# Kernel tuning notes

Hardware: AMD Instinct MI355X
Metric: run time of the kernel (lower is better)

## Reference

```python
import jax, jax.numpy as jnp
import numpy as np

STRIDES = (8, 16, 32, 64, 128)
LEVEL_HW = ((128, 160), (64, 80), (32, 40), (16, 20), (8, 10))
IMG_H, IMG_W = 1024, 1280
B, NUM_CLASSES = 16, 20
SCORE_THR, IOU_THR, MAX_DET = 0.05, 0.6, 1000


def _coords_all():
    # coords_fmap2orig for every level, concatenated -> [N, 2] (x, y)
    cs = []
    for (h, w), s in zip(LEVEL_HW, STRIDES):
        sx = jnp.arange(w, dtype=jnp.float32) * s + s // 2
        sy = jnp.arange(h, dtype=jnp.float32) * s + s // 2
        yy, xx = jnp.meshgrid(sy, sx, indexing='ij')
        cs.append(jnp.stack([xx.reshape(-1), yy.reshape(-1)], -1))
    return jnp.concatenate(cs, 0)


def _reshape_cat(levels):
    # list of [B,C,h,w] -> [B, sum(h*w), C]
    return jnp.concatenate(
        [p.transpose(0, 2, 3, 1).reshape(p.shape[0], -1, p.shape[1]) for p in levels], 1)


def _decode(cls_l, cnt_l, reg_l, coords):
    cls = jax.nn.sigmoid(_reshape_cat(cls_l))           # [B,N,C]
    cnt = jax.nn.sigmoid(_reshape_cat(cnt_l))[..., 0]   # [B,N]
    reg = _reshape_cat(reg_l)                           # [B,N,4] ltrb
    scores = jnp.sqrt(jnp.max(cls, -1) * cnt)           # add_centerness + sqrt
    classes = jnp.argmax(cls, -1) + 1
    boxes = jnp.concatenate([coords[None] - reg[..., :2], coords[None] + reg[..., 2:]], -1)
    return scores, classes, boxes


def _nms_keep(boxes, scores, classes, valid):
    # masked greedy per-class NMS on fixed size M; returns keep mask [M]
    boxes = jax.lax.stop_gradient(boxes)
    scores = jax.lax.stop_gradient(scores)
    maxc = jnp.max(jnp.where(valid[:, None], boxes, 0.0))
    b = boxes + (classes.astype(boxes.dtype) * (maxc + 1.0))[:, None]  # class offsets
    order = jnp.argsort(-jnp.where(valid, scores, -jnp.inf))
    b = b[order]
    v = valid[order]
    x1, y1, x2, y2 = b[:, 0], b[:, 1], b[:, 2], b[:, 3]
    areas = (x2 - x1 + 1.0) * (y2 - y1 + 1.0)
    iw = jnp.clip(jnp.minimum(x2[:, None], x2[None, :]) - jnp.maximum(x1[:, None], x1[None, :]) + 1.0, 0.0)
    ih = jnp.clip(jnp.minimum(y2[:, None], y2[None, :]) - jnp.maximum(y1[:, None], y1[None, :]) + 1.0, 0.0)
    inter = iw * ih
    iou = inter / (areas[:, None] + areas[None, :] - inter)
    M = boxes.shape[0]

    def body(i, carry):
        keep, sup = carry
        k = v[i] & (~sup[i])
        keep = keep.at[i].set(k)
        sup = sup | (k & (iou[i] > IOU_THR))
        return keep, sup

    keep_s, _ = jax.lax.fori_loop(0, M, body, (jnp.zeros(M, bool), jnp.zeros(M, bool)))
    return jnp.zeros(M, bool).at[order].set(keep_s)


def _forward(args):
    cls_r, cnt_r, reg_r = args[0:5], args[5:10], args[10:15]
    cls_i, cnt_i, reg_i = args[15:20], args[20:25], args[25:30]
    coords = _coords_all()
    s_r, c_r, b_r = _decode(cls_r, cnt_r, reg_r, coords)
    s_i, c_i, b_i = _decode(cls_i, cnt_i, reg_i, coords)
    scores = jnp.concatenate([s_r, s_i], 1)   # [B, 2N]
    classes = jnp.concatenate([c_r, c_i], 1)
    boxes = jnp.concatenate([b_r, b_i], 1)
    top_s, top_i = jax.lax.top_k(scores, MAX_DET)
    top_c = jnp.take_along_axis(classes, top_i, 1)
    top_b = jnp.take_along_axis(boxes, top_i[..., None], 1)
    valid = top_s >= SCORE_THR
    keep = jax.vmap(_nms_keep)(top_b, top_s, top_c, valid)
    # ClipBoxes: clamp to image bounds
    top_b = jnp.maximum(top_b, 0.0)
    xs = jnp.minimum(top_b[..., 0::2], IMG_W - 1.0)
    ys = jnp.minimum(top_b[..., 1::2], IMG_H - 1.0)
    top_b = jnp.stack([xs[..., 0], ys[..., 0], xs[..., 1], ys[..., 1]], -1)
    kf = keep.astype(top_s.dtype)
    return top_s * kf, top_c * keep, top_b * kf[..., None], keep


def setup_inputs() -> dict:
    key = jax.random.key(0)
    chans = {'cls': NUM_CLASSES, 'cnt': 1, 'reg': 4}
    inp = {}
    i = 0
    for mod in ('r', 'i'):
        for kind in ('cls', 'cnt', 'reg'):
            for l, (h, w) in enumerate(LEVEL_HW):
                k = jax.random.fold_in(key, i); i += 1
                inp[f'{kind}_{mod}_{l}'] = jax.random.normal(k, (B, chans[kind], h, w), jnp.float32)
    return inp


def reference(cls_r_0, cls_r_1, cls_r_2, cls_r_3, cls_r_4,
              cnt_r_0, cnt_r_1, cnt_r_2, cnt_r_3, cnt_r_4,
              reg_r_0, reg_r_1, reg_r_2, reg_r_3, reg_r_4,
              cls_i_0, cls_i_1, cls_i_2, cls_i_3, cls_i_4,
              cnt_i_0, cnt_i_1, cnt_i_2, cnt_i_3, cnt_i_4,
              reg_i_0, reg_i_1, reg_i_2, reg_i_3, reg_i_4):
    args = [cls_r_0, cls_r_1, cls_r_2, cls_r_3, cls_r_4,
            cnt_r_0, cnt_r_1, cnt_r_2, cnt_r_3, cnt_r_4,
            reg_r_0, reg_r_1, reg_r_2, reg_r_3, reg_r_4,
            cls_i_0, cls_i_1, cls_i_2, cls_i_3, cls_i_4,
            cnt_i_0, cnt_i_1, cnt_i_2, cnt_i_3, cnt_i_4,
            reg_i_0, reg_i_1, reg_i_2, reg_i_3, reg_i_4]
    return _forward(args)
```

## Files before the change

kernel.cpp:

```cpp
#include <hip/hip_runtime.h>
#include <hip/hip_bf16.h>

typedef unsigned long long u64;
typedef unsigned int u32;

#define NTOT    54560
#define NMOD    27280
#define BATCH   16
#define KPAD    1024
#define MAXD    1000
#define NBIN    16384
#define CAND    6144
#define NCHUNK  7

struct Ptrs { const float* p[30]; };

constexpr size_t SZ_KEY    = (size_t)BATCH * NTOT * 8;
constexpr size_t SZ_TOPK   = (size_t)BATCH * KPAD * 8;
constexpr size_t SZ_TRAW   = (size_t)BATCH * KPAD * 16;
constexpr size_t SZ_T1     = (size_t)BATCH * KPAD * 4;
constexpr size_t SZ_MAXC   = (size_t)BATCH * 32 * 4;
constexpr size_t SZ_VALID  = (size_t)BATCH * 32 * 4;
constexpr size_t SZ_MASK   = (size_t)BATCH * KPAD * 32 * 4;
constexpr size_t SZ_GHIST  = (size_t)BATCH * NBIN * 4;
constexpr size_t SZ_GHISTP = (size_t)BATCH * NCHUNK * NBIN * 4;
constexpr size_t SZ_GB1    = 256;
constexpr size_t SZ_GCAND  = (size_t)BATCH * CAND * 8;

constexpr size_t OFF_KEY    = 0;
constexpr size_t OFF_TOPK   = OFF_KEY   + SZ_KEY;
constexpr size_t OFF_TRAW   = OFF_TOPK  + SZ_TOPK;
constexpr size_t OFF_TSCORE = OFF_TRAW  + SZ_TRAW;
constexpr size_t OFF_TCLSF  = OFF_TSCORE+ SZ_T1;
constexpr size_t OFF_MAXC   = OFF_TCLSF + SZ_T1;
constexpr size_t OFF_VALID  = OFF_MAXC  + SZ_MAXC;
constexpr size_t OFF_MASK   = OFF_VALID + SZ_VALID;
constexpr size_t OFF_GHIST  = OFF_MASK  + SZ_MASK;
constexpr size_t OFF_GHISTP = OFF_GHIST + SZ_GHIST;
constexpr size_t OFF_GB1    = OFF_GHISTP+ SZ_GHISTP;
constexpr size_t OFF_GCAND  = OFF_GB1   + SZ_GB1;

__device__ inline void level_of(int nm, int& l, int& pos, int& w, int& s, int& hw) {
    if (nm < 20480)      { l = 0; pos = nm;         w = 160; s = 8;   hw = 20480; }
    else if (nm < 25600) { l = 1; pos = nm - 20480; w = 80;  s = 16;  hw = 5120; }
    else if (nm < 26880) { l = 2; pos = nm - 25600; w = 40;  s = 32;  hw = 1280; }
    else if (nm < 27200) { l = 3; pos = nm - 26880; w = 20;  s = 64;  hw = 320; }
    else                 { l = 4; pos = nm - 27200; w = 10;  s = 128; hw = 80; }
}

__device__ inline float sigm(float x) { return 1.0f / (1.0f + expf(-x)); }

__device__ inline void ld_lds16(const float* g, float* l) {
    __builtin_amdgcn_global_load_lds(
        (const __attribute__((address_space(1))) void*)g,
        (__attribute__((address_space(3))) void*)l, 16, 0, 0);
}

__global__ __launch_bounds__(128)
void decode_kernel(Ptrs ptrs, u64* __restrict__ keyAll) {
    __shared__ float lds[21 * 512];
    int cc = blockIdx.x;
    int b = blockIdx.y;

    if (cc >= 100) {
        int t = (cc - 100) * 128 + threadIdx.x;
        if (t >= 3360) return;
        int mod = t / 1680;
        int tm = t % 1680;
        int q = t & 3;
        int nm = 25600 + (tm & ~3);
        int l, pos, w, s, hw;
        level_of(nm, l, pos, w, s, hw);
        (void)w; (void)s;
        const float* clsP = ptrs.p[mod * 15 + l];
        const float* cntP = ptrs.p[mod * 15 + 5 + l];
        const float4* cb = (const float4*)(clsP + (size_t)b * 20 * hw + pos);
        int hw4 = hw >> 2;
        int c0 = q * 5;
        float4 v[5];
        #pragma unroll
        for (int c = 0; c < 5; ++c) v[c] = cb[(size_t)(c0 + c) * hw4];
        float4 cv = *(const float4*)(cntP + (size_t)b * hw + pos);
        float4 mx = v[0];
        #pragma unroll
        for (int c = 1; c < 5; ++c) {
            mx.x = fmaxf(mx.x, v[c].x); mx.y = fmaxf(mx.y, v[c].y);
            mx.z = fmaxf(mx.z, v[c].z); mx.w = fmaxf(mx.w, v[c].w);
        }
        mx.x = fmaxf(mx.x, __shfl_xor(mx.x, 1));
        mx.y = fmaxf(mx.y, __shfl_xor(mx.y, 1));
        mx.z = fmaxf(mx.z, __shfl_xor(mx.z, 1));
        mx.w = fmaxf(mx.w, __shfl_xor(mx.w, 1));
        mx.x = fmaxf(mx.x, __shfl_xor(mx.x, 2));
        mx.y = fmaxf(mx.y, __shfl_xor(mx.y, 2));
        mx.z = fmaxf(mx.z, __shfl_xor(mx.z, 2));
        mx.w = fmaxf(mx.w, __shfl_xor(mx.w, 2));
        float ma = (q & 1) ? ((q & 2) ? mx.w : mx.y) : ((q & 2) ? mx.z : mx.x);
        float ca = (q & 1) ? ((q & 2) ? cv.w : cv.y) : ((q & 2) ? cv.z : cv.x);
        u32 sb = __float_as_uint(sqrtf(__fmul_rn(sigm(ma), sigm(ca))));
        int n = mod * NMOD + nm + q;
        keyAll[(size_t)b * NTOT + n] = ((u64)sb << 16) | (u64)(65535 - n);
        return;
    }

    int mod = cc / 50, c = cc % 50;
    int l     = (c < 40) ? 0 : 1;
    int hw    = (c < 40) ? 20480 : 5120;
    int pos0  = (c < 40) ? c * 512 : (c - 40) * 512;
    int nmb   = (l == 0) ? pos0 : 20480 + pos0;
    const float* clsP = ptrs.p[mod * 15 + l];
    const float* cntP = ptrs.p[mod * 15 + 5 + l];
    int wave = threadIdx.x >> 6, lane = threadIdx.x & 63;

    const float* cbase = clsP + (size_t)b * 20 * hw + pos0 + wave * 256 + lane * 4;
    float* dbase = lds + wave * 256;
    #pragma unroll
    for (int ch = 0; ch < 20; ++ch)
        ld_lds16(cbase + (size_t)ch * hw, dbase + ch * 512);
    ld_lds16(cntP + (size_t)b * hw + pos0 + wave * 256 + lane * 4, dbase + 20 * 512);
    __syncthreads();

    int t = threadIdx.x;
    const float4* l4 = (const float4*)lds;
    float4 mx = l4[t];
    #pragma unroll
    for (int ch = 1; ch < 20; ++ch) {
        float4 v = l4[ch * 128 + t];
        mx.x = fmaxf(mx.x, v.x); mx.y = fmaxf(mx.y, v.y);
        mx.z = fmaxf(mx.z, v.z); mx.w = fmaxf(mx.w, v.w);
    }
    float4 cv = l4[20 * 128 + t];

    int n = mod * NMOD + nmb + t * 4;
    u32 s0 = __float_as_uint(sqrtf(__fmul_rn(sigm(mx.x), sigm(cv.x))));
    u32 s1 = __float_as_uint(sqrtf(__fmul_rn(sigm(mx.y), sigm(cv.y))));
    u32 s2 = __float_as_uint(sqrtf(__fmul_rn(sigm(mx.z), sigm(cv.z))));
    u32 s3 = __float_as_uint(sqrtf(__fmul_rn(sigm(mx.w), sigm(cv.w))));
    ulonglong2* ka2 = (ulonglong2*)(keyAll + (size_t)b * NTOT + n);
    ulonglong2 k01, k23;
    k01.x = ((u64)s0 << 16) | (u64)(65535 - n);
    k01.y = ((u64)s1 << 16) | (u64)(65535 - (n + 1));
    k23.x = ((u64)s2 << 16) | (u64)(65535 - (n + 2));
    k23.y = ((u64)s3 << 16) | (u64)(65535 - (n + 3));
    ka2[0] = k01; ka2[1] = k23;
}

__global__ __launch_bounds__(1024)
void hist_kernel(const u64* __restrict__ keyAll, u32* __restrict__ ghistP,
                 u32* __restrict__ maxcG) {
    __shared__ u32 shist[NBIN];
    int b = blockIdx.y, chunk = blockIdx.x, tid = threadIdx.x;
    #pragma unroll
    for (int j = 0; j < NBIN / 1024; ++j) shist[tid + j * 1024] = 0u;
    if (chunk == 0 && tid == 0) maxcG[b * 32] = 0u;
    __syncthreads();

    const u64* keys = keyAll + (size_t)b * NTOT;
    int n0 = chunk * 8192;
    u64 kk[8];
    #pragma unroll
    for (int r = 0; r < 8; ++r) {
        int idx = n0 + r * 1024 + tid;
        kk[r] = (idx < NTOT) ? keys[idx] : ~0ull;
    }
    #pragma unroll
    for (int r = 0; r < 8; ++r)
        if (kk[r] != ~0ull) atomicAdd(&shist[(u32)(kk[r] >> 32)], 1u);
    __syncthreads();

    u32* gp = ghistP + ((size_t)b * NCHUNK + chunk) * NBIN;
    #pragma unroll
    for (int j = 0; j < NBIN / 1024; ++j) gp[tid + j * 1024] = shist[tid + j * 1024];
}

__global__ __launch_bounds__(1024)
void scan_kernel(const u32* __restrict__ ghistP, u32* __restrict__ ghist,
                 int* __restrict__ gB1) {
    __shared__ u32 shist[NBIN];
    __shared__ u32 warep[16];
    __shared__ int sB1;
    int b = blockIdx.x, tid = threadIdx.x;
    int lane = tid & 63, wid = tid >> 6;

    const u32* gp = ghistP + (size_t)b * NCHUNK * NBIN;
    for (int i = tid; i < NBIN; i += 1024) {
        u32 s = 0;
        #pragma unroll
        for (int c = 0; c < NCHUNK; ++c) s += gp[(size_t)c * NBIN + i];
        shist[i] = s;
    }
    __syncthreads();

    u32 loc[16]; u32 sum = 0;
    #pragma unroll
    for (int j = 0; j < 16; ++j) { loc[j] = shist[NBIN - 1 - (tid * 16 + j)]; sum += loc[j]; }
    u32 v = sum;
    #pragma unroll
    for (int off = 1; off < 64; off <<= 1) {
        u32 t2 = (u32)__shfl_up((int)v, off);
        if (lane >= off) v += t2;
    }
    if (lane == 63) warep[wid] = v;
    __syncthreads();
    if (tid < 16) {
        u32 p = warep[tid];
        #pragma unroll
        for (int off = 1; off < 16; off <<= 1) {
            u32 t2 = (u32)__shfl_up((int)p, off);
            if (tid >= off) p += t2;
        }
        warep[tid] = p;
    }
    __syncthreads();
    u32 incl = v + (wid ? warep[wid - 1] : 0u);
    u32 excl = incl - sum;
    if (excl < (u32)MAXD && incl >= (u32)MAXD) {
        u32 c = excl;
        #pragma unroll
        for (int j = 0; j < 16; ++j) {
            c += loc[j];
            if (c >= (u32)MAXD) { sB1 = NBIN - 1 - (tid * 16 + j); break; }
        }
    }
    u32 run = excl;
    #pragma unroll
    for (int j = 0; j < 16; ++j) {
        int bin = NBIN - 1 - (tid * 16 + j);
        shist[bin] = run;
        run += loc[j];
    }
    __syncthreads();

    u32* gh = ghist + (size_t)b * NBIN;
    for (int i = tid; i < NBIN; i += 1024) gh[i] = shist[i];
    if (tid == 0) gB1[b] = sB1;
}

__global__ __launch_bounds__(1024)
void scatter_kernel(const u64* __restrict__ keyAll, u32* __restrict__ ghist,
                    const int* __restrict__ gB1, u64* __restrict__ gcand) {
    int b = blockIdx.y, tid = threadIdx.x;
    int n0 = blockIdx.x * 8192;
    int B1 = gB1[b];
    const u64* keys = keyAll + (size_t)b * NTOT;
    u32* gh = ghist + (size_t)b * NBIN;
    u64* gc = gcand + (size_t)b * CAND;
    u64 kk[8];
    #pragma unroll
    for (int r = 0; r < 8; ++r) {
        int idx = n0 + r * 1024 + tid;
        kk[r] = (idx < NTOT) ? keys[idx] : 0ull;
    }
    #pragma unroll
    for (int r = 0; r < 8; ++r) {
        if (kk[r] != 0ull && (int)(kk[r] >> 32) >= B1) {
            u32 p = atomicAdd(&gh[(u32)(kk[r] >> 32)], 1u);
            if (p < CAND) gc[p] = kk[r];
        }
    }
}

__global__ __launch_bounds__(1024)
void fixup_kernel(const u64* __restrict__ gcand, const u32* __restrict__ ghist,
                  const int* __restrict__ gB1, u64* __restrict__ topkey) {
    __shared__ u64 scand[CAND];
    __shared__ u64 stopk[KPAD];
    int b = blockIdx.x, tid = threadIdx.x;
    const u32* gh = ghist + (size_t)b * NBIN;
    int B1 = gB1[b];
    int Ctot = min((int)gh[B1], CAND);
    for (int i = tid; i < Ctot; i += 1024) scand[i] = gcand[(size_t)b * CAND + i];
    __syncthreads();
    for (int i = tid; i < Ctot; i += 1024) {
        u64 ki = scand[i];
        int bin = (int)(ki >> 32);
        int st = (int)gh[bin + 1];
        int en = min((int)gh[bin], Ctot);
        int pos = st;
        for (int j = st; j < en; ++j) pos += (scand[j] > ki) ? 1 : 0;
        if (pos < MAXD) stopk[pos] = ki;
    }
    __syncthreads();
    if (tid < MAXD) topkey[(size_t)b * KPAD + tid] = stopk[tid];
}

__global__ __launch_bounds__(128)
void gather_kernel(Ptrs ptrs, const u64* __restrict__ topkey,
                   float4* __restrict__ traw, float* __restrict__ tscore,
                   float* __restrict__ tclsf, u32* __restrict__ validwords,
                   u32* __restrict__ maxcG) {
    #pragma clang fp contract(off)
    int b = blockIdx.y;
    int tid = threadIdx.x;
    int half = tid & 1;
    int i = blockIdx.x * 64 + (tid >> 1);
    int active = (i < MAXD);

    float score = 0.f;
    float best = -1.0f; int bi = 0;
    float ra = 0.f, rb2 = 0.f;
    int pos = 0, w = 1, s = 0;
    if (active) {
        u64 key = topkey[(size_t)b * KPAD + i];
        int n = 65535 - (int)(key & 0xFFFFull);
        score = __uint_as_float((u32)(key >> 16));
        int mod = (n >= NMOD) ? 1 : 0;
        int nm = n - mod * NMOD;
        int l, hw;
        level_of(nm, l, pos, w, s, hw);
        const float* clsP = ptrs.p[mod * 15 + l];
        const float* regP = ptrs.p[mod * 15 + 10 + l];
        const float* cbp = clsP + (size_t)b * 20 * hw + pos;
        const float* rbp = regP + (size_t)b * 4 * hw + pos;
        float cl[10];
        int c0 = half * 10;
        #pragma unroll
        for (int c = 0; c < 10; ++c) cl[c] = cbp[(size_t)(c0 + c) * hw];
        ra  = rbp[(size_t)(half * 2) * hw];
        rb2 = rbp[(size_t)(half * 2 + 1) * hw];
        #pragma unroll
        for (int c = 0; c < 10; ++c) {
            float p = sigm(cl[c]);
            if (p > best) { best = p; bi = c0 + c; }
        }
    }
    float po  = __shfl_xor(best, 1);
    int   bio = __shfl_xor(bi, 1);
    float rao = __shfl_xor(ra, 1);
    float rbo = __shfl_xor(rb2, 1);
    if (half == 0) { if (po > best)  { best = po; bi = bio; } }
    else           { if (po >= best) { best = po; bi = bio; } }
    float clsf = active ? (float)(bi + 1) : 0.f;
    float r0 = half ? rao : ra,  r1 = half ? rbo : rb2;
    float r2 = half ? ra  : rao, r3 = half ? rb2 : rbo;

    float4 bx = make_float4(0.f, 0.f, 0.f, 0.f);
    if (active) {
        int xi = pos % w, yi = pos / w;
        float cx = (float)(xi * s + (s >> 1));
        float cy = (float)(yi * s + (s >> 1));
        bx.x = cx - r0; bx.y = cy - r1; bx.z = cx + r2; bx.w = cy + r3;
    }
    int valid = active && (score >= 0.05f) && (half == 0);
    float contrib = valid ? fmaxf(0.0f, fmaxf(fmaxf(bx.x, bx.y), fmaxf(bx.z, bx.w))) : 0.0f;
    float red = contrib;
    #pragma unroll
    for (int off = 32; off > 0; off >>= 1) red = fmaxf(red, __shfl_down(red, off));
    if ((tid & 63) == 0) atomicMax(&maxcG[b * 32], __float_as_uint(red));
    u64 ball = __ballot(valid != 0);
    if ((tid & 63) == 0) {
        u32 word = 0;
        for (int j = 0; j < 32; ++j) word |= (u32)((ball >> (2 * j)) & 1ull) << j;
        validwords[b * 32 + blockIdx.x * 2 + (tid >> 6)] = word;
    }
    if (half == 0) {
        size_t oo = (size_t)b * KPAD + i;
        traw[oo] = bx; tscore[oo] = score; tclsf[oo] = clsf;
    }
}

#define SW(t) ((((t) & 31) << 3) | ((t) >> 5))
__global__ __launch_bounds__(256)
void mask_kernel(const float4* __restrict__ traw, const float* __restrict__ tclsf,
                 const u32* __restrict__ maxcG, u32* __restrict__ maskG) {
    #pragma clang fp contract(off)
    int u = blockIdx.x, b = blockIdx.y, tid = threadIdx.x;
    int g, wg;
    if (u < 32)      { g = u >> 2;              wg = u & 3; }
    else if (u < 56) { int d = u - 32; g = 8  + d / 3;        wg = 1 + d % 3; }
    else if (u < 72) { int d = u - 56; g = 16 + (d >> 1);     wg = 2 + (d & 1); }
    else             { g = 24 + (u - 72);       wg = 3; }
    int i0 = g * 32, j0 = wg * 256;
    float m1 = __uint_as_float(maxcG[b * 32]) + 1.0f;

    __shared__ float cx1[256], cy1[256], cx2[256], cy2[256], ca[256];
    {
        int t = tid;
        float4 f = traw[(size_t)b * KPAD + j0 + t];
        float o = __fmul_rn(tclsf[(size_t)b * KPAD + j0 + t], m1);
        float ox1 = __fadd_rn(f.x, o), oy1 = __fadd_rn(f.y, o);
        float ox2 = __fadd_rn(f.z, o), oy2 = __fadd_rn(f.w, o);
        float dw = ox2 - ox1 + 1.0f;
        float dh = oy2 - oy1 + 1.0f;
        int ts = SW(t);
        cx1[ts] = ox1; cy1[ts] = oy1; cx2[ts] = ox2; cy2[ts] = oy2;
        ca[ts] = __fmul_rn(dw, dh);
    }
    __syncthreads();

    int ir = tid >> 3, wr = tid & 7;
    int i = i0 + ir;
    float4 fi = traw[(size_t)b * KPAD + i];
    float oi = __fmul_rn(tclsf[(size_t)b * KPAD + i], m1);
    float ix1 = __fadd_rn(fi.x, oi), iy1 = __fadd_rn(fi.y, oi);
    float ix2 = __fadd_rn(fi.z, oi), iy2 = __fadd_rn(fi.w, oi);
    float dwi = ix2 - ix1 + 1.0f, dhi = iy2 - iy1 + 1.0f;
    float ai = __fmul_rn(dwi, dhi);
    u32 bits = 0;
    int jb = wr * 32;
    for (int jj = 0; jj < 32; ++jj) {
        int js = SW(jb + jj);
        float iw = fminf(ix2, cx2[js]) - fmaxf(ix1, cx1[js]) + 1.0f;
        iw = fmaxf(iw, 0.0f);
        float ih = fminf(iy2, cy2[js]) - fmaxf(iy1, cy1[js]) + 1.0f;
        ih = fmaxf(ih, 0.0f);
        float inter = iw * ih;
        float denom = (ai + ca[js]) - inter;
        float iou = inter / denom;
        bits |= (iou > 0.6f) ? (1u << jj) : 0u;
    }
    maskG[((size_t)b * KPAD + i) * 32 + wg * 8 + wr] = bits;
}

__global__ __launch_bounds__(512)
void scan_out_kernel(const u32* __restrict__ maskG, const u32* __restrict__ validbits,
                     const float4* __restrict__ traw, const float* __restrict__ tscore,
                     const float* __restrict__ tclsf, float* __restrict__ out) {
    __shared__ u32 sm[KPAD * 32];
    __shared__ u32 keeps[32];
    int b = blockIdx.x, tid = threadIdx.x;

    const uint4* s4 = (const uint4*)(maskG + (size_t)b * KPAD * 32);
    uint4* d4 = (uint4*)sm;
    #pragma unroll
    for (int r = 0; r < 16; ++r) {
        int w4 = tid + r * 512;
        int row = w4 >> 3, c4 = w4 & 7;
        d4[(row << 3) | (c4 ^ (row & 7))] = s4[w4];
    }
    __syncthreads();

    if (tid < 64) {
        int lane = tid, lw = lane & 31;
        int rbase = (lane >> 5) << 4;
        u32 vword = validbits[b * 32 + lw];
        u32 removed = 0u, keepw = 0u;
        for (int g = 0; g < 32; ++g) {
            int i0 = g << 5;
            u32 intra = sm[((i0 + lw) << 5) | (g ^ ((lw & 7) << 2))];
            u32 remg = (u32)__builtin_amdgcn_readlane((int)removed, g);
            u32 valg = (u32)__builtin_amdgcn_readlane((int)vword, g);
            u32 cand = valg & ~remg;
            u32 keep32 = 0u, sup = 0u;
            #pragma unroll
            for (int i = 0; i < 32; ++i) {
                u32 mi = (u32)__builtin_amdgcn_readlane((int)intra, i);
                u32 kb = cand & ~sup & (1u << i);
                sup |= kb ? mi : 0u;
                keep32 |= kb;
            }
            u32 ksh = keep32 >> rbase;
            u32 acc0 = 0u, acc1 = 0u;
            #pragma unroll
            for (int r = 0; r < 16; r += 2) {
                u32 r0 = sm[((i0 + rbase + r)     << 5) | (lw ^ ((r & 7) << 2))];
                u32 r1 = sm[((i0 + rbase + r + 1) << 5) | (lw ^ (((r + 1) & 7) << 2))];
                acc0 |= ((ksh >> r) & 1u)       ? r0 : 0u;
                acc1 |= ((ksh >> (r + 1)) & 1u) ? r1 : 0u;
            }
            u32 acc = acc0 | acc1;
            acc |= (u32)__shfl_xor((int)acc, 32);
            removed |= acc;
            if (lw == g) keepw = keep32;
        }
        if (lane < 32) keeps[lw] = keepw;
    }
    __syncthreads();

    const int BQ = BATCH * MAXD;
    for (int s2 = tid; s2 < MAXD; s2 += 512) {
        u32 kf = (keeps[s2 >> 5] >> (s2 & 31)) & 1u;
        size_t oo = (size_t)b * KPAD + s2;
        float score = tscore[oo];
        float clsf = tclsf[oo];
        float4 bx = traw[oo];
        float x1 = fminf(fmaxf(bx.x, 0.f), 1279.f);
        float y1 = fminf(fmaxf(bx.y, 0.f), 1023.f);
        float x2 = fminf(fmaxf(bx.z, 0.f), 1279.f);
        float y2 = fminf(fmaxf(bx.w, 0.f), 1023.f);
        int base = b * MAXD + s2;
        out[base] = kf ? score : 0.0f;
        out[BQ + base] = kf ? clsf : 0.0f;
        float* ob = out + 2 * BQ + (size_t)base * 4;
        ob[0] = kf ? x1 : 0.f; ob[1] = kf ? y1 : 0.f;
        ob[2] = kf ? x2 : 0.f; ob[3] = kf ? y2 : 0.f;
        out[6 * BQ + base] = kf ? 1.0f : 0.0f;
    }
}

extern "C" void kernel_launch(void* const* d_in, const int* in_sizes, int n_in,
                              void* d_out, int out_size, void* d_ws, size_t ws_size,
                              hipStream_t stream) {
    Ptrs ptrs;
    for (int i = 0; i < 30; ++i) ptrs.p[i] = (const float*)d_in[i];

    char* ws = (char*)d_ws;
    u64*    keyAll    = (u64*)   (ws + OFF_KEY);
    u64*    topkey    = (u64*)   (ws + OFF_TOPK);
    float4* traw      = (float4*)(ws + OFF_TRAW);
    float*  tscore    = (float*) (ws + OFF_TSCORE);
    float*  tclsf     = (float*) (ws + OFF_TCLSF);
    u32*    maxcG     = (u32*)   (ws + OFF_MAXC);
    u32*    validbits = (u32*)   (ws + OFF_VALID);
    u32*    maskG     = (u32*)   (ws + OFF_MASK);
    u32*    ghist     = (u32*)   (ws + OFF_GHIST);
    u32*    ghistP    = (u32*)   (ws + OFF_GHISTP);
    int*    gB1       = (int*)   (ws + OFF_GB1);
    u64*    gcand     = (u64*)   (ws + OFF_GCAND);
    float*  out       = (float*)d_out;

    decode_kernel<<<dim3(127, BATCH), 128, 0, stream>>>(ptrs, keyAll);
    hist_kernel<<<dim3(NCHUNK, BATCH), 1024, 0, stream>>>(keyAll, ghistP, maxcG);
    scan_kernel<<<BATCH, 1024, 0, stream>>>(ghistP, ghist, gB1);
    scatter_kernel<<<dim3(NCHUNK, BATCH), 1024, 0, stream>>>(keyAll, ghist, gB1, gcand);
    fixup_kernel<<<BATCH, 1024, 0, stream>>>(gcand, ghist, gB1, topkey);
    gather_kernel<<<dim3(16, BATCH), 128, 0, stream>>>(ptrs, topkey, traw, tscore, tclsf,
                                                       validbits, maxcG);
    mask_kernel<<<dim3(80, BATCH), 256, 0, stream>>>(traw, tclsf, maxcG, maskG);
    scan_out_kernel<<<BATCH, 512, 0, stream>>>(maskG, validbits, traw, tscore, tclsf, out);
}
```

Before: 246.6 us.

## Simplify decode to per-thread float4 loads and split histogram merge from scan

The decode kernel drops its LDS staging path (global_load_lds plus barrier) and its separate small-level path. Instead, each thread directly loads 20 class channels and the centerness as float4 across all levels, with a flat 256-thread grid. The chunk-histogram merge moves out of the 16-block scan kernel into a separate merge kernel with 8x16 blocks, so the 7-way reduction over 16384 bins runs on many more CUs. The scan then reads and writes global memory directly, at the cost of one extra launch and global rather than LDS traffic.

Result: slower. 254.7 us (+3.3%).

```diff
diff --git a/kernel.cpp b/kernel.cpp
--- a/kernel.cpp
+++ b/kernel.cpp
@@ -50,88 +50,31 @@
 
 __device__ inline float sigm(float x) { return 1.0f / (1.0f + expf(-x)); }
 
-__device__ inline void ld_lds16(const float* g, float* l) {
-    __builtin_amdgcn_global_load_lds(
-        (const __attribute__((address_space(1))) void*)g,
-        (__attribute__((address_space(3))) void*)l, 16, 0, 0);
-}
-
-__global__ __launch_bounds__(128)
+__global__ __launch_bounds__(256)
 void decode_kernel(Ptrs ptrs, u64* __restrict__ keyAll) {
-    __shared__ float lds[21 * 512];
-    int cc = blockIdx.x;
     int b = blockIdx.y;
-
-    if (cc >= 100) {
-        int t = (cc - 100) * 128 + threadIdx.x;
-        if (t >= 3360) return;
-        int mod = t / 1680;
-        int tm = t % 1680;
-        int q = t & 3;
-        int nm = 25600 + (tm & ~3);
-        int l, pos, w, s, hw;
-        level_of(nm, l, pos, w, s, hw);
-        (void)w; (void)s;
-        const float* clsP = ptrs.p[mod * 15 + l];
-        const float* cntP = ptrs.p[mod * 15 + 5 + l];
-        const float4* cb = (const float4*)(clsP + (size_t)b * 20 * hw + pos);
-        int hw4 = hw >> 2;
-        int c0 = q * 5;
-        float4 v[5];
-        #pragma unroll
-        for (int c = 0; c < 5; ++c) v[c] = cb[(size_t)(c0 + c) * hw4];
-        float4 cv = *(const float4*)(cntP + (size_t)b * hw + pos);
-        float4 mx = v[0];
-        #pragma unroll
-        for (int c = 1; c < 5; ++c) {
-            mx.x = fmaxf(mx.x, v[c].x); mx.y = fmaxf(mx.y, v[c].y);
-            mx.z = fmaxf(mx.z, v[c].z); mx.w = fmaxf(mx.w, v[c].w);
-        }
-        mx.x = fmaxf(mx.x, __shfl_xor(mx.x, 1));
-        mx.y = fmaxf(mx.y, __shfl_xor(mx.y, 1));
-        mx.z = fmaxf(mx.z, __shfl_xor(mx.z, 1));
-        mx.w = fmaxf(mx.w, __shfl_xor(mx.w, 1));
-        mx.x = fmaxf(mx.x, __shfl_xor(mx.x, 2));
-        mx.y = fmaxf(mx.y, __shfl_xor(mx.y, 2));
-        mx.z = fmaxf(mx.z, __shfl_xor(mx.z, 2));
-        mx.w = fmaxf(mx.w, __shfl_xor(mx.w, 2));
-        float ma = (q & 1) ? ((q & 2) ? mx.w : mx.y) : ((q & 2) ? mx.z : mx.x);
-        float ca = (q & 1) ? ((q & 2) ? cv.w : cv.y) : ((q & 2) ? cv.z : cv.x);
-        u32 sb = __float_as_uint(sqrtf(__fmul_rn(sigm(ma), sigm(ca))));
-        int n = mod * NMOD + nm + q;
-        keyAll[(size_t)b * NTOT + n] = ((u64)sb << 16) | (u64)(65535 - n);
-        return;
-    }
-
-    int mod = cc / 50, c = cc % 50;
-    int l     = (c < 40) ? 0 : 1;
-    int hw    = (c < 40) ? 20480 : 5120;
-    int pos0  = (c < 40) ? c * 512 : (c - 40) * 512;
-    int nmb   = (l == 0) ? pos0 : 20480 + pos0;
+    int gid = blockIdx.x * 256 + threadIdx.x;
+    if (gid >= 13640) return;
+    int mod = (gid >= 6820) ? 1 : 0;
+    int nm = (mod ? gid - 6820 : gid) * 4;
+    int l, pos, w, s, hw;
+    level_of(nm, l, pos, w, s, hw);
+    (void)w; (void)s;
     const float* clsP = ptrs.p[mod * 15 + l];
     const float* cntP = ptrs.p[mod * 15 + 5 + l];
-    int wave = threadIdx.x >> 6, lane = threadIdx.x & 63;
-
-    const float* cbase = clsP + (size_t)b * 20 * hw + pos0 + wave * 256 + lane * 4;
-    float* dbase = lds + wave * 256;
-    #pragma unroll
-    for (int ch = 0; ch < 20; ++ch)
-        ld_lds16(cbase + (size_t)ch * hw, dbase + ch * 512);
-    ld_lds16(cntP + (size_t)b * hw + pos0 + wave * 256 + lane * 4, dbase + 20 * 512);
-    __syncthreads();
-
-    int t = threadIdx.x;
-    const float4* l4 = (const float4*)lds;
-    float4 mx = l4[t];
-    #pragma unroll
-    for (int ch = 1; ch < 20; ++ch) {
-        float4 v = l4[ch * 128 + t];
+    const float4* cb = (const float4*)(clsP + (size_t)b * 20 * hw + pos);
+    int hw4 = hw >> 2;
+
+    float4 mx = cb[0];
+    #pragma unroll
+    for (int c = 1; c < 20; ++c) {
+        float4 v = cb[(size_t)c * hw4];
         mx.x = fmaxf(mx.x, v.x); mx.y = fmaxf(mx.y, v.y);
         mx.z = fmaxf(mx.z, v.z); mx.w = fmaxf(mx.w, v.w);
     }
-    float4 cv = l4[20 * 128 + t];
-
-    int n = mod * NMOD + nmb + t * 4;
+    float4 cv = *(const float4*)(cntP + (size_t)b * hw + pos);
+
+    int n = mod * NMOD + nm;
     u32 s0 = __float_as_uint(sqrtf(__fmul_rn(sigm(mx.x), sigm(cv.x))));
     u32 s1 = __float_as_uint(sqrtf(__fmul_rn(sigm(mx.y), sigm(cv.y))));
     u32 s2 = __float_as_uint(sqrtf(__fmul_rn(sigm(mx.z), sigm(cv.z))));
@@ -173,27 +116,30 @@
     for (int j = 0; j < NBIN / 1024; ++j) gp[tid + j * 1024] = shist[tid + j * 1024];
 }
 
-__global__ __launch_bounds__(1024)
-void scan_kernel(const u32* __restrict__ ghistP, u32* __restrict__ ghist,
-                 int* __restrict__ gB1) {
-    __shared__ u32 shist[NBIN];
-    __shared__ u32 warep[16];
-    __shared__ int sB1;
-    int b = blockIdx.x, tid = threadIdx.x;
-    int lane = tid & 63, wid = tid >> 6;
-
-    const u32* gp = ghistP + (size_t)b * NCHUNK * NBIN;
-    for (int i = tid; i < NBIN; i += 1024) {
+__global__ __launch_bounds__(256)
+void merge_kernel(const u32* __restrict__ ghistP, u32* __restrict__ ghist) {
+    int b = blockIdx.y, m = blockIdx.x, tid = threadIdx.x;
+    const u32* gp = ghistP + (size_t)b * NCHUNK * NBIN + m * 2048;
+    u32* gh = ghist + (size_t)b * NBIN + m * 2048;
+    for (int i = tid; i < 2048; i += 256) {
         u32 s = 0;
         #pragma unroll
         for (int c = 0; c < NCHUNK; ++c) s += gp[(size_t)c * NBIN + i];
-        shist[i] = s;
-    }
-    __syncthreads();
+        gh[i] = s;
+    }
+}
+
+__global__ __launch_bounds__(1024)
+void scan_kernel(u32* __restrict__ ghist, int* __restrict__ gB1) {
+    int b = blockIdx.x, tid = threadIdx.x;
+    int lane = tid & 63, wid = tid >> 6;
+    __shared__ u32 warep[16];
+    __shared__ int sB1;
+    u32* gh = ghist + (size_t)b * NBIN;
 
     u32 loc[16]; u32 sum = 0;
     #pragma unroll
-    for (int j = 0; j < 16; ++j) { loc[j] = shist[NBIN - 1 - (tid * 16 + j)]; sum += loc[j]; }
+    for (int j = 0; j < 16; ++j) { loc[j] = gh[NBIN - 1 - (tid * 16 + j)]; sum += loc[j]; }
     u32 v = sum;
     #pragma unroll
     for (int off = 1; off < 64; off <<= 1) {
@@ -226,13 +172,10 @@
     #pragma unroll
     for (int j = 0; j < 16; ++j) {
         int bin = NBIN - 1 - (tid * 16 + j);
-        shist[bin] = run;
+        gh[bin] = run;
         run += loc[j];
     }
     __syncthreads();
-
-    u32* gh = ghist + (size_t)b * NBIN;
-    for (int i = tid; i < NBIN; i += 1024) gh[i] = shist[i];
     if (tid == 0) gB1[b] = sB1;
 }
 
@@ -509,9 +452,10 @@
     u64*    gcand     = (u64*)   (ws + OFF_GCAND);
     float*  out       = (float*)d_out;
 
-    decode_kernel<<<dim3(127, BATCH), 128, 0, stream>>>(ptrs, keyAll);
+    decode_kernel<<<dim3(54, BATCH), 256, 0, stream>>>(ptrs, keyAll);
     hist_kernel<<<dim3(NCHUNK, BATCH), 1024, 0, stream>>>(keyAll, ghistP, maxcG);
-    scan_kernel<<<BATCH, 1024, 0, stream>>>(ghistP, ghist, gB1);
+    merge_kernel<<<dim3(8, BATCH), 256, 0, stream>>>(ghistP, ghist);
+    scan_kernel<<<BATCH, 1024, 0, stream>>>(ghist, gB1);
     scatter_kernel<<<dim3(NCHUNK, BATCH), 1024, 0, stream>>>(keyAll, ghist, gB1, gcand);
     fixup_kernel<<<BATCH, 1024, 0, stream>>>(gcand, ghist, gB1, topkey);
     gather_kernel<<<dim3(16, BATCH), 128, 0, stream>>>(ptrs, topkey, traw, tscore, tclsf,
```
